# Kernel tuning notes

Hardware: AMD Instinct MI355X
Metric: run time of the kernel (lower is better)

Reference implementation:

```python
import jax, jax.numpy as jnp
import numpy as np

N_QUBITS = 4
N_QLAYERS = 2
NOISE = 0.05
LN_EPS = 1e-5
C64 = jnp.complex64

PX = jnp.array([[0, 1], [1, 0]], C64)
PY = jnp.array([[0, -1j], [1j, 0]], C64)
PZ = jnp.array([[1, 0], [0, -1]], C64)
CNOT = jnp.array([[1, 0, 0, 0], [0, 1, 0, 0], [0, 0, 0, 1], [0, 0, 1, 0]], C64).reshape(2, 2, 2, 2)


def _rx(t):
    c = jnp.cos(t / 2).astype(C64)
    s = jnp.sin(t / 2).astype(C64)
    return jnp.stack([jnp.stack([c, -1j * s], -1), jnp.stack([-1j * s, c], -1)], -2)


def _ry(t):
    c = jnp.cos(t / 2).astype(C64)
    s = jnp.sin(t / 2).astype(C64)
    return jnp.stack([jnp.stack([c, -s], -1), jnp.stack([s, c], -1)], -2)


def _rz(t):
    e = jnp.exp(-0.5j * t.astype(C64))
    z = jnp.zeros_like(e)
    return jnp.stack([jnp.stack([e, z], -1), jnp.stack([z, jnp.conj(e)], -1)], -2)


def _apply_1q(rho, U, q):
    # rho: [B] + [2]*8 (row qubit axes 1..4, col qubit axes 5..8); U: [2,2] or [B,2,2]
    r = jnp.moveaxis(rho, 1 + q, 1)
    r = jnp.einsum('bij,bj...->bi...', U, r) if U.ndim == 3 else jnp.einsum('ij,bj...->bi...', U, r)
    r = jnp.moveaxis(r, 1, 1 + q)
    r = jnp.moveaxis(r, 5 + q, -1)
    Uc = jnp.conj(U)
    r = jnp.einsum('b...j,bij->b...i', r, Uc) if U.ndim == 3 else jnp.einsum('b...j,ij->b...i', r, Uc)
    return jnp.moveaxis(r, -1, 5 + q)


def _apply_cnot(rho, c, t):
    r = jnp.moveaxis(rho, (1 + c, 1 + t), (1, 2))
    r = jnp.einsum('ABij,bij...->bAB...', CNOT, r)
    r = jnp.moveaxis(r, (1, 2), (1 + c, 1 + t))
    r = jnp.moveaxis(r, (5 + c, 5 + t), (-2, -1))
    r = jnp.einsum('b...ij,ABij->b...AB', r, jnp.conj(CNOT))
    return jnp.moveaxis(r, (-2, -1), (5 + c, 5 + t))


def _depolarize_all(rho, p):
    # rho -> (1-p) rho + p/3 (X rho X + Y rho Y + Z rho Z) on every qubit
    for q in range(N_QUBITS):
        rho = (1 - p) * rho + (p / 3) * (_apply_1q(rho, PX, q) + _apply_1q(rho, PY, q) + _apply_1q(rho, PZ, q))
    return rho


def _circuit(angles, w):
    # angles: [B,4] float, w: [2,4] float -> expval PauliZ per qubit: [B,4] float
    B = angles.shape[0]
    rho = jnp.zeros((B, 16, 16), C64).at[:, 0, 0].set(1.0).reshape((B,) + (2,) * 8)
    for i in range(N_QUBITS):
        rho = _apply_1q(rho, _rx(angles[:, i]), i)
        rho = _apply_1q(rho, _rz(angles[:, i]), i)
    for i in range(N_QUBITS):
        rho = _apply_1q(rho, _rx(w[0, i]), i)
        rho = _apply_1q(rho, _rz(w[1, i]), i)
    if NOISE > 0:
        rho = _depolarize_all(rho, NOISE)
    for l in range(1, N_QLAYERS):
        for i in range(N_QUBITS):
            rho = _apply_cnot(rho, i, (i + 1) % N_QUBITS)
            rho = _apply_1q(rho, _ry(w[l, i]), i)
            rho = _apply_1q(rho, _rz(w[l, i]), i)
        if NOISE > 0:
            rho = _depolarize_all(rho, NOISE)
    diag = jnp.real(jnp.diagonal(rho.reshape(B, 16, 16), axis1=1, axis2=2))  # [B,16]
    bits = (jnp.arange(16)[:, None] >> jnp.arange(N_QUBITS - 1, -1, -1)[None, :]) & 1
    signs = (1 - 2 * bits).astype(jnp.float32)  # [16,4]
    return diag @ signs


def setup_inputs() -> dict:
    key = jax.random.key(0)
    ks = jax.random.split(key, 4)
    B, D = 65536, 256
    x = jax.random.normal(ks[0], (B, D), jnp.float32)
    W_in = jax.random.normal(ks[1], (N_QUBITS, D), jnp.float32) * (1.0 / np.sqrt(D))
    b_in = jnp.zeros((N_QUBITS,), jnp.float32)
    gamma = jnp.ones((N_QUBITS,), jnp.float32)
    beta = jnp.zeros((N_QUBITS,), jnp.float32)
    qweights = jax.random.uniform(ks[2], (N_QLAYERS, N_QUBITS), jnp.float32, 0.0, 2.0 * np.pi)
    W_out = jax.random.normal(ks[3], (D, N_QUBITS), jnp.float32) * 0.5
    b_out = jnp.zeros((D,), jnp.float32)
    return dict(x=x, W_in=W_in, b_in=b_in, gamma=gamma, beta=beta, qweights=qweights, W_out=W_out, b_out=b_out)


def reference(x, W_in, b_in, gamma, beta, qweights, W_out, b_out):
    xp = jnp.tanh(x @ W_in.T + b_in)
    mu = jnp.mean(xp, -1, keepdims=True)
    var = jnp.mean((xp - mu) ** 2, -1, keepdims=True)
    angles = (xp - mu) / jnp.sqrt(var + LN_EPS) * gamma + beta  # timestep = 0.0
    z = _circuit(angles, qweights)
    out = z @ W_out.T + b_out
    return x + out  # residual: input_dim == output_dim
```

## Files before the change

### kernel.cpp

```cpp
#include <hip/hip_runtime.h>
#include <math.h>

#define DIM 256

__global__ void qc_setup_kernel(const float* __restrict__ qw, float* __restrict__ T)
{
  __shared__ float Vr[16][16], Vi[16][16];
  __shared__ float Or[16][16], Oi[16][16];
  const int tid = threadIdx.x;
  const int r = tid >> 4, c = tid & 15;

  Vr[r][c] = (r == c) ? 1.0f : 0.0f;
  Vi[r][c] = 0.0f;
  __syncthreads();

  #pragma unroll 1
  for (int i = 0; i < 4; ++i) {
    const int cm = 8 >> i;
    const int tm = 8 >> ((i + 1) & 3);
    {
      const int k = (r & cm) ? (r ^ tm) : r;
      const float nr = Vr[k][c], ni = Vi[k][c];
      __syncthreads();
      Vr[r][c] = nr; Vi[r][c] = ni;
      __syncthreads();
    }
    const float w  = qw[4 + i];
    const float ch = cosf(0.5f * w), sh = sinf(0.5f * w);
    {
      const int m = 8 >> i;
      const int r0 = r & ~m, r1 = r | m;
      float u0, u1;
      if (r & m) { u0 = sh; u1 = ch; } else { u0 = ch; u1 = -sh; }
      const float nr = u0 * Vr[r0][c] + u1 * Vr[r1][c];
      const float ni = u0 * Vi[r0][c] + u1 * Vi[r1][c];
      __syncthreads();
      Vr[r][c] = nr; Vi[r][c] = ni;
      __syncthreads();
    }
    {
      const int m = 8 >> i;
      const float pr = ch;
      const float pi = (r & m) ? sh : -sh;
      const float vr = Vr[r][c], vi = Vi[r][c];
      Vr[r][c] = pr * vr - pi * vi;
      Vi[r][c] = pr * vi + pi * vr;
      __syncthreads();
    }
  }

  const int q  = blockIdx.x;
  const int zm = 8 >> q;
  float orr = 0.0f, oii = 0.0f;
  for (int k = 0; k < 16; ++k) {
    const float sgn = (k & zm) ? -1.0f : 1.0f;
    const float ar = Vr[k][r], ai = -Vi[k][r];
    const float br = Vr[k][c], bi = Vi[k][c];
    orr += sgn * (ar * br - ai * bi);
    oii += sgn * (ar * bi + ai * br);
  }
  __syncthreads();
  Or[r][c] = orr; Oi[r][c] = oii;
  __syncthreads();

  const float sdep = 1.0f - 4.0f * 0.05f / 3.0f;
  const int p0 = tid >> 6, p1 = (tid >> 4) & 3, p2 = (tid >> 2) & 3, p3 = tid & 3;
  float tr = 0.0f;
  for (int n = 0; n < 16; ++n) {
    int m = n;
    float fr = 1.0f, fi = 0.0f;
    #pragma unroll
    for (int i2 = 0; i2 < 4; ++i2) {
      const int a   = (n >> (3 - i2)) & 1;
      const int pi_ = (i2 == 0) ? p0 : (i2 == 1) ? p1 : (i2 == 2) ? p2 : p3;
      if (pi_ == 1) {
        m ^= (8 >> i2);
      } else if (pi_ == 2) {
        m ^= (8 >> i2);
        const float s2  = a ? 1.0f : -1.0f;
        const float nfr = -fi * s2, nfi = fr * s2;
        fr = nfr; fi = nfi;
      } else if (pi_ == 3) {
        if (a) { fr = -fr; fi = -fi; }
      }
    }
    tr += fr * Or[m][n] - fi * Oi[m][n];
  }
  const int nnz = (p0 != 0) + (p1 != 0) + (p2 != 0) + (p3 != 0);
  float scale = 1.0f / 16.0f;
  for (int e = 0; e <= nnz; ++e) scale *= sdep;
  T[q * 256 + tid] = tr * scale;
}

__global__ __launch_bounds__(512)
__attribute__((amdgpu_waves_per_eu(4, 8)))
void qlayer_main_kernel(
    const float* __restrict__ x,
    const float* __restrict__ Win,
    const float* __restrict__ b_in,
    const float* __restrict__ gamma,
    const float* __restrict__ beta,
    const float* __restrict__ qw,
    const float* __restrict__ Wout,
    const float* __restrict__ b_out,
    const float* __restrict__ M,
    float* __restrict__ out,
    int B)
{
  __shared__ float accs[64][4];
  __shared__ float zz[64][4];

  const int tid  = threadIdx.x;
  const int lane = tid & 63;
  const int wv   = tid >> 6;
  const int lrow0 = wv * 8;
  const size_t grow0 = (size_t)blockIdx.x * 64 + lrow0;

  float4 winf[4];
  #pragma unroll
  for (int q = 0; q < 4; ++q)
    winf[q] = *reinterpret_cast<const float4*>(&Win[q * 256 + lane * 4]);

  float4 xr[8];
  #pragma unroll
  for (int i = 0; i < 8; ++i)
    xr[i] = *reinterpret_cast<const float4*>(&x[(grow0 + i) * DIM + lane * 4]);

  #pragma unroll
  for (int p = 0; p < 4; ++p) {
    float aA[4], aB[4];
    const float4 xa = xr[p * 2], xb = xr[p * 2 + 1];
    #pragma unroll
    for (int q = 0; q < 4; ++q) {
      aA[q] = xa.x * winf[q].x + xa.y * winf[q].y + xa.z * winf[q].z + xa.w * winf[q].w;
      aB[q] = xb.x * winf[q].x + xb.y * winf[q].y + xb.z * winf[q].z + xb.w * winf[q].w;
    }
    #pragma unroll
    for (int q = 0; q < 4; ++q) {
      aA[q] += __shfl_xor(aA[q], 32, 64);
      aB[q] += __shfl_xor(aB[q], 32, 64);
      aA[q] = (lane < 32) ? aA[q] : aB[q];
    }
    #pragma unroll
    for (int off = 1; off < 32; off <<= 1) {
      #pragma unroll
      for (int q = 0; q < 4; ++q) aA[q] += __shfl_xor(aA[q], off, 64);
    }
    if ((lane & 31) == 0) {
      const int lr = lrow0 + p * 2 + (lane >> 5);
      *reinterpret_cast<float4*>(&accs[lr][0]) = make_float4(aA[0], aA[1], aA[2], aA[3]);
    }
  }
  __syncthreads();

  if (tid < 64) {
    const float4 av = *reinterpret_cast<const float4*>(&accs[tid][0]);
    const float aq[4] = {av.x, av.y, av.z, av.w};

    float xp[4];
    #pragma unroll
    for (int q = 0; q < 4; ++q) {
      const float e = __expf(2.0f * (aq[q] + b_in[q]));
      xp[q] = 1.0f - __fdividef(2.0f, e + 1.0f);
    }
    const float mu = 0.25f * (xp[0] + xp[1] + xp[2] + xp[3]);
    const float d0 = xp[0] - mu, d1 = xp[1] - mu, d2 = xp[2] - mu, d3 = xp[3] - mu;
    const float var = 0.25f * (d0 * d0 + d1 * d1 + d2 * d2 + d3 * d3);
    const float inv = rsqrtf(var + 1e-5f);

    float A0[4], A1[4], A2[4], A3[4];
    #pragma unroll
    for (int i = 0; i < 4; ++i) {
      const float w0 = qw[i], w1 = qw[4 + i];
      const float cwa = cosf(w0), swa = sinf(w0);
      const float cwb = cosf(w1), swb = sinf(w1);
      const float ang = ((i == 0 ? d0 : i == 1 ? d1 : i == 2 ? d2 : d3) * inv) * gamma[i] + beta[i];
      float sn, cs;
      __sincosf(ang, &sn, &cs);
      const float ax = sn * sn;
      const float ay = -sn * cs;
      const float az = cs;
      const float ay2 = ay * cwa - az * swa;
      const float az2 = ay * swa + az * cwa;
      const float Axv = ax * cwb - ay2 * swb;
      const float Ayv = ax * swb + ay2 * cwb;
      float* dst = (i == 0) ? A0 : (i == 1) ? A1 : (i == 2) ? A2 : A3;
      dst[0] = 1.0f; dst[1] = Axv; dst[2] = Ayv; dst[3] = az2;
    }

    float v[16];
    #pragma unroll
    for (int a = 0; a < 4; ++a)
      #pragma unroll
      for (int b = 0; b < 4; ++b)
        v[a * 4 + b] = A2[a] * A3[b];

    float z[4];
    #pragma unroll
    for (int q = 0; q < 4; ++q) {
      float zq = 0.0f;
      #pragma unroll
      for (int j = 0; j < 16; ++j) {
        const float* Mr = &M[(q * 16 + j) * 16];
        float w = 0.0f;
        #pragma unroll
        for (int k = 0; k < 16; ++k) w += Mr[k] * v[k];
        zq += (A0[j >> 2] * A1[j & 3]) * w;
      }
      z[q] = zq;
    }
    *reinterpret_cast<float4*>(&zz[tid][0]) = make_float4(z[0], z[1], z[2], z[3]);
  }
  __syncthreads();

  float4 woutf[4];
  #pragma unroll
  for (int j = 0; j < 4; ++j)
    woutf[j] = *reinterpret_cast<const float4*>(&Wout[(lane * 4 + j) * 4]);
  const float4 boutf = *reinterpret_cast<const float4*>(&b_out[lane * 4]);

  #pragma unroll
  for (int i = 0; i < 8; ++i) {
    const float4 zv = *reinterpret_cast<const float4*>(&zz[lrow0 + i][0]);
    const float4 xv = xr[i];
    float4 o;
    o.x = xv.x + boutf.x + zv.x * woutf[0].x + zv.y * woutf[0].y + zv.z * woutf[0].z + zv.w * woutf[0].w;
    o.y = xv.y + boutf.y + zv.x * woutf[1].x + zv.y * woutf[1].y + zv.z * woutf[1].z + zv.w * woutf[1].w;
    o.z = xv.z + boutf.z + zv.x * woutf[2].x + zv.y * woutf[2].y + zv.z * woutf[2].z + zv.w * woutf[2].w;
    o.w = xv.w + boutf.w + zv.x * woutf[3].x + zv.y * woutf[3].y + zv.z * woutf[3].z + zv.w * woutf[3].w;
    *reinterpret_cast<float4*>(&out[(grow0 + i) * DIM + lane * 4]) = o;
  }
}

extern "C" void kernel_launch(void* const* d_in, const int* in_sizes, int n_in,
                              void* d_out, int out_size, void* d_ws, size_t ws_size,
                              hipStream_t stream)
{
  const float* x     = (const float*)d_in[0];
  const float* Win   = (const float*)d_in[1];
  const float* b_in  = (const float*)d_in[2];
  const float* gamma = (const float*)d_in[3];
  const float* beta  = (const float*)d_in[4];
  const float* qw    = (const float*)d_in[5];
  const float* Wout  = (const float*)d_in[6];
  const float* b_out = (const float*)d_in[7];
  float* out = (float*)d_out;
  float* T   = (float*)d_ws;
  const int B = in_sizes[0] / DIM;

  hipLaunchKernelGGL(qc_setup_kernel, dim3(4), dim3(256), 0, stream, qw, T);

  const int nblocks = B / 64;
  hipLaunchKernelGGL(qlayer_main_kernel, dim3(nblocks), dim3(512), 0, stream,
                     x, Win, b_in, gamma, beta, qw, Wout, b_out, T, out, B);
}
```

Measured before the change: 53.40 us.

## Split fused main kernel into projection, circuit, and epilogue kernels

New measurement: 64.66 us. 21.1% more time.

```diff
diff --git a/kernel.cpp b/kernel.cpp
--- a/kernel.cpp
+++ b/kernel.cpp
@@ -92,144 +92,152 @@
   T[q * 256 + tid] = tr * scale;
 }
 
-__global__ __launch_bounds__(512)
-__attribute__((amdgpu_waves_per_eu(4, 8)))
-void qlayer_main_kernel(
+__global__ __launch_bounds__(256) void k1_angles(
     const float* __restrict__ x,
     const float* __restrict__ Win,
+    float* __restrict__ acc,
+    int B)
+{
+  const int lane = threadIdx.x & 63;
+  const int wid  = blockIdx.x * (blockDim.x >> 6) + (threadIdx.x >> 6);
+  const int nw   = gridDim.x * (blockDim.x >> 6);
+
+  float4 winf[4];
+  #pragma unroll
+  for (int q = 0; q < 4; ++q)
+    winf[q] = *reinterpret_cast<const float4*>(&Win[q * 256 + lane * 4]);
+
+  const int npair = B >> 1;
+  #pragma unroll 1
+  for (int p = wid; p < npair; p += nw) {
+    const size_t base = (size_t)p * 2 * DIM + lane * 4;
+    const float4 xa = *reinterpret_cast<const float4*>(&x[base]);
+    const float4 xb = *reinterpret_cast<const float4*>(&x[base + DIM]);
+
+    float aA[4], aB[4];
+    #pragma unroll
+    for (int q = 0; q < 4; ++q) {
+      aA[q] = xa.x * winf[q].x + xa.y * winf[q].y + xa.z * winf[q].z + xa.w * winf[q].w;
+      aB[q] = xb.x * winf[q].x + xb.y * winf[q].y + xb.z * winf[q].z + xb.w * winf[q].w;
+    }
+    #pragma unroll
+    for (int q = 0; q < 4; ++q) {
+      aA[q] += __shfl_xor(aA[q], 32, 64);
+      aB[q] += __shfl_xor(aB[q], 32, 64);
+      aA[q] = (lane < 32) ? aA[q] : aB[q];
+    }
+    #pragma unroll
+    for (int off = 1; off < 32; off <<= 1) {
+      #pragma unroll
+      for (int q = 0; q < 4; ++q) aA[q] += __shfl_xor(aA[q], off, 64);
+    }
+    if ((lane & 31) == 0) {
+      const int row = p * 2 + (lane >> 5);
+      *reinterpret_cast<float4*>(&acc[(size_t)row * 4]) =
+          make_float4(aA[0], aA[1], aA[2], aA[3]);
+    }
+  }
+}
+
+__global__ __launch_bounds__(256) void k2_middle(
+    const float* __restrict__ acc,
     const float* __restrict__ b_in,
     const float* __restrict__ gamma,
     const float* __restrict__ beta,
     const float* __restrict__ qw,
+    const float* __restrict__ M,
+    float* __restrict__ z,
+    int B)
+{
+  const int g = blockIdx.x * blockDim.x + threadIdx.x;
+  if (g >= B) return;
+
+  const float4 av = *reinterpret_cast<const float4*>(&acc[(size_t)g * 4]);
+  const float aq[4] = {av.x, av.y, av.z, av.w};
+
+  float xp[4];
+  #pragma unroll
+  for (int q = 0; q < 4; ++q) {
+    const float e = __expf(2.0f * (aq[q] + b_in[q]));
+    xp[q] = 1.0f - __fdividef(2.0f, e + 1.0f);
+  }
+  const float mu = 0.25f * (xp[0] + xp[1] + xp[2] + xp[3]);
+  const float d0 = xp[0] - mu, d1 = xp[1] - mu, d2 = xp[2] - mu, d3 = xp[3] - mu;
+  const float var = 0.25f * (d0 * d0 + d1 * d1 + d2 * d2 + d3 * d3);
+  const float inv = rsqrtf(var + 1e-5f);
+
+  float A0[4], A1[4], A2[4], A3[4];
+  #pragma unroll
+  for (int i = 0; i < 4; ++i) {
+    const float w0 = qw[i], w1 = qw[4 + i];
+    const float cwa = cosf(w0), swa = sinf(w0);
+    const float cwb = cosf(w1), swb = sinf(w1);
+    const float ang = ((i == 0 ? d0 : i == 1 ? d1 : i == 2 ? d2 : d3) * inv) * gamma[i] + beta[i];
+    float sn, cs;
+    __sincosf(ang, &sn, &cs);
+    const float ax = sn * sn;
+    const float ay = -sn * cs;
+    const float az = cs;
+    const float ay2 = ay * cwa - az * swa;
+    const float az2 = ay * swa + az * cwa;
+    const float Axv = ax * cwb - ay2 * swb;
+    const float Ayv = ax * swb + ay2 * cwb;
+    float* dst = (i == 0) ? A0 : (i == 1) ? A1 : (i == 2) ? A2 : A3;
+    dst[0] = 1.0f; dst[1] = Axv; dst[2] = Ayv; dst[3] = az2;
+  }
+
+  float v[16];
+  #pragma unroll
+  for (int a = 0; a < 4; ++a)
+    #pragma unroll
+    for (int b = 0; b < 4; ++b)
+      v[a * 4 + b] = A2[a] * A3[b];
+
+  float zo[4];
+  #pragma unroll
+  for (int q = 0; q < 4; ++q) {
+    float zq = 0.0f;
+    #pragma unroll
+    for (int j = 0; j < 16; ++j) {
+      const float* Mr = &M[(q * 16 + j) * 16];
+      float w = 0.0f;
+      #pragma unroll
+      for (int k = 0; k < 16; ++k) w += Mr[k] * v[k];
+      zq += (A0[j >> 2] * A1[j & 3]) * w;
+    }
+    zo[q] = zq;
+  }
+  *reinterpret_cast<float4*>(&z[(size_t)g * 4]) =
+      make_float4(zo[0], zo[1], zo[2], zo[3]);
+}
+
+__global__ __launch_bounds__(256) void k3_epilogue(
+    const float* __restrict__ x,
+    const float* __restrict__ z,
     const float* __restrict__ Wout,
     const float* __restrict__ b_out,
-    const float* __restrict__ M,
     float* __restrict__ out,
     int B)
 {
-  __shared__ float accs[64][4];
-  __shared__ float zz[64][4];
-
-  const int tid  = threadIdx.x;
-  const int lane = tid & 63;
-  const int wv   = tid >> 6;
-  const int lrow0 = wv * 8;
-  const size_t grow0 = (size_t)blockIdx.x * 64 + lrow0;
-
-  float4 winf[4];
-  #pragma unroll
-  for (int q = 0; q < 4; ++q)
-    winf[q] = *reinterpret_cast<const float4*>(&Win[q * 256 + lane * 4]);
-
-  float4 xr[8];
-  #pragma unroll
-  for (int i = 0; i < 8; ++i)
-    xr[i] = *reinterpret_cast<const float4*>(&x[(grow0 + i) * DIM + lane * 4]);
-
-  #pragma unroll
-  for (int p = 0; p < 4; ++p) {
-    float aA[4], aB[4];
-    const float4 xa = xr[p * 2], xb = xr[p * 2 + 1];
-    #pragma unroll
-    for (int q = 0; q < 4; ++q) {
-      aA[q] = xa.x * winf[q].x + xa.y * winf[q].y + xa.z * winf[q].z + xa.w * winf[q].w;
-      aB[q] = xb.x * winf[q].x + xb.y * winf[q].y + xb.z * winf[q].z + xb.w * winf[q].w;
-    }
-    #pragma unroll
-    for (int q = 0; q < 4; ++q) {
-      aA[q] += __shfl_xor(aA[q], 32, 64);
-      aB[q] += __shfl_xor(aB[q], 32, 64);
-      aA[q] = (lane < 32) ? aA[q] : aB[q];
-    }
-    #pragma unroll
-    for (int off = 1; off < 32; off <<= 1) {
-      #pragma unroll
-      for (int q = 0; q < 4; ++q) aA[q] += __shfl_xor(aA[q], off, 64);
-    }
-    if ((lane & 31) == 0) {
-      const int lr = lrow0 + p * 2 + (lane >> 5);
-      *reinterpret_cast<float4*>(&accs[lr][0]) = make_float4(aA[0], aA[1], aA[2], aA[3]);
-    }
-  }
-  __syncthreads();
-
-  if (tid < 64) {
-    const float4 av = *reinterpret_cast<const float4*>(&accs[tid][0]);
-    const float aq[4] = {av.x, av.y, av.z, av.w};
-
-    float xp[4];
-    #pragma unroll
-    for (int q = 0; q < 4; ++q) {
-      const float e = __expf(2.0f * (aq[q] + b_in[q]));
-      xp[q] = 1.0f - __fdividef(2.0f, e + 1.0f);
-    }
-    const float mu = 0.25f * (xp[0] + xp[1] + xp[2] + xp[3]);
-    const float d0 = xp[0] - mu, d1 = xp[1] - mu, d2 = xp[2] - mu, d3 = xp[3] - mu;
-    const float var = 0.25f * (d0 * d0 + d1 * d1 + d2 * d2 + d3 * d3);
-    const float inv = rsqrtf(var + 1e-5f);
-
-    float A0[4], A1[4], A2[4], A3[4];
-    #pragma unroll
-    for (int i = 0; i < 4; ++i) {
-      const float w0 = qw[i], w1 = qw[4 + i];
-      const float cwa = cosf(w0), swa = sinf(w0);
-      const float cwb = cosf(w1), swb = sinf(w1);
-      const float ang = ((i == 0 ? d0 : i == 1 ? d1 : i == 2 ? d2 : d3) * inv) * gamma[i] + beta[i];
-      float sn, cs;
-      __sincosf(ang, &sn, &cs);
-      const float ax = sn * sn;
-      const float ay = -sn * cs;
-      const float az = cs;
-      const float ay2 = ay * cwa - az * swa;
-      const float az2 = ay * swa + az * cwa;
-      const float Axv = ax * cwb - ay2 * swb;
-      const float Ayv = ax * swb + ay2 * cwb;
-      float* dst = (i == 0) ? A0 : (i == 1) ? A1 : (i == 2) ? A2 : A3;
-      dst[0] = 1.0f; dst[1] = Axv; dst[2] = Ayv; dst[3] = az2;
-    }
-
-    float v[16];
-    #pragma unroll
-    for (int a = 0; a < 4; ++a)
-      #pragma unroll
-      for (int b = 0; b < 4; ++b)
-        v[a * 4 + b] = A2[a] * A3[b];
-
-    float z[4];
-    #pragma unroll
-    for (int q = 0; q < 4; ++q) {
-      float zq = 0.0f;
-      #pragma unroll
-      for (int j = 0; j < 16; ++j) {
-        const float* Mr = &M[(q * 16 + j) * 16];
-        float w = 0.0f;
-        #pragma unroll
-        for (int k = 0; k < 16; ++k) w += Mr[k] * v[k];
-        zq += (A0[j >> 2] * A1[j & 3]) * w;
-      }
-      z[q] = zq;
-    }
-    *reinterpret_cast<float4*>(&zz[tid][0]) = make_float4(z[0], z[1], z[2], z[3]);
-  }
-  __syncthreads();
-
-  float4 woutf[4];
-  #pragma unroll
-  for (int j = 0; j < 4; ++j)
-    woutf[j] = *reinterpret_cast<const float4*>(&Wout[(lane * 4 + j) * 4]);
-  const float4 boutf = *reinterpret_cast<const float4*>(&b_out[lane * 4]);
-
-  #pragma unroll
-  for (int i = 0; i < 8; ++i) {
-    const float4 zv = *reinterpret_cast<const float4*>(&zz[lrow0 + i][0]);
-    const float4 xv = xr[i];
-    float4 o;
-    o.x = xv.x + boutf.x + zv.x * woutf[0].x + zv.y * woutf[0].y + zv.z * woutf[0].z + zv.w * woutf[0].w;
-    o.y = xv.y + boutf.y + zv.x * woutf[1].x + zv.y * woutf[1].y + zv.z * woutf[1].z + zv.w * woutf[1].w;
-    o.z = xv.z + boutf.z + zv.x * woutf[2].x + zv.y * woutf[2].y + zv.z * woutf[2].z + zv.w * woutf[2].w;
-    o.w = xv.w + boutf.w + zv.x * woutf[3].x + zv.y * woutf[3].y + zv.z * woutf[3].z + zv.w * woutf[3].w;
-    *reinterpret_cast<float4*>(&out[(grow0 + i) * DIM + lane * 4]) = o;
-  }
+  const size_t g = (size_t)blockIdx.x * blockDim.x + threadIdx.x;
+  const int row = (int)(g >> 6);
+  const int c4  = (int)(g & 63);
+  if (row >= B) return;
+
+  const float4 xv = *reinterpret_cast<const float4*>(&x[g * 4]);
+  const float4 zv = *reinterpret_cast<const float4*>(&z[(size_t)row * 4]);
+  const float4 w0 = *reinterpret_cast<const float4*>(&Wout[(c4 * 4 + 0) * 4]);
+  const float4 w1 = *reinterpret_cast<const float4*>(&Wout[(c4 * 4 + 1) * 4]);
+  const float4 w2 = *reinterpret_cast<const float4*>(&Wout[(c4 * 4 + 2) * 4]);
+  const float4 w3 = *reinterpret_cast<const float4*>(&Wout[(c4 * 4 + 3) * 4]);
+  const float4 bv = *reinterpret_cast<const float4*>(&b_out[c4 * 4]);
+
+  float4 o;
+  o.x = xv.x + bv.x + zv.x * w0.x + zv.y * w0.y + zv.z * w0.z + zv.w * w0.w;
+  o.y = xv.y + bv.y + zv.x * w1.x + zv.y * w1.y + zv.z * w1.z + zv.w * w1.w;
+  o.z = xv.z + bv.z + zv.x * w2.x + zv.y * w2.y + zv.z * w2.z + zv.w * w2.w;
+  o.w = xv.w + bv.w + zv.x * w3.x + zv.y * w3.y + zv.z * w3.z + zv.w * w3.w;
+  *reinterpret_cast<float4*>(&out[g * 4]) = o;
 }
 
 extern "C" void kernel_launch(void* const* d_in, const int* in_sizes, int n_in,
@@ -245,12 +253,20 @@
   const float* Wout  = (const float*)d_in[6];
   const float* b_out = (const float*)d_in[7];
   float* out = (float*)d_out;
-  float* T   = (float*)d_ws;
   const int B = in_sizes[0] / DIM;
 
-  hipLaunchKernelGGL(qc_setup_kernel, dim3(4), dim3(256), 0, stream, qw, T);
-
-  const int nblocks = B / 64;
-  hipLaunchKernelGGL(qlayer_main_kernel, dim3(nblocks), dim3(512), 0, stream,
-                     x, Win, b_in, gamma, beta, qw, Wout, b_out, T, out, B);
-}
+  float* M   = (float*)d_ws;
+  float* acc = M + 1024;
+  float* zbuf = acc + (size_t)B * 4;
+
+  hipLaunchKernelGGL(qc_setup_kernel, dim3(4), dim3(256), 0, stream, qw, M);
+
+  hipLaunchKernelGGL(k1_angles, dim3(2048), dim3(256), 0, stream, x, Win, acc, B);
+
+  hipLaunchKernelGGL(k2_middle, dim3((B + 255) / 256), dim3(256), 0, stream,
+                     acc, b_in, gamma, beta, qw, M, zbuf, B);
+
+  const size_t nf4 = (size_t)B * 64;
+  hipLaunchKernelGGL(k3_epilogue, dim3((unsigned)((nf4 + 255) / 256)), dim3(256),
+                     0, stream, x, zbuf, Wout, b_out, out, B);
+}
```

## Stage x tile transposed in shared memory and compute input projection per-thread

Applied to the files above, without the earlier changes.

New measurement: 70.15 us. +31.4%, slower.

```diff
diff --git a/kernel.cpp b/kernel.cpp
--- a/kernel.cpp
+++ b/kernel.cpp
@@ -2,6 +2,7 @@
 #include <math.h>
 
 #define DIM 256
+#define TILE 32
 
 __global__ void qc_setup_kernel(const float* __restrict__ qw, float* __restrict__ T)
 {
@@ -92,9 +93,7 @@
   T[q * 256 + tid] = tr * scale;
 }
 
-__global__ __launch_bounds__(512)
-__attribute__((amdgpu_waves_per_eu(4, 8)))
-void qlayer_main_kernel(
+__global__ __launch_bounds__(256) void qlayer_main_kernel(
     const float* __restrict__ x,
     const float* __restrict__ Win,
     const float* __restrict__ b_in,
@@ -107,60 +106,46 @@
     float* __restrict__ out,
     int B)
 {
-  __shared__ float accs[64][4];
-  __shared__ float zz[64][4];
+  __shared__ float xs[256][33];
+  __shared__ float accs[32][4];
+  __shared__ float zz[32][4];
 
   const int tid  = threadIdx.x;
+  const int w    = tid >> 6;
   const int lane = tid & 63;
-  const int wv   = tid >> 6;
-  const int lrow0 = wv * 8;
-  const size_t grow0 = (size_t)blockIdx.x * 64 + lrow0;
-
-  float4 winf[4];
+  const int r0   = blockIdx.x * TILE;
+
   #pragma unroll
-  for (int q = 0; q < 4; ++q)
-    winf[q] = *reinterpret_cast<const float4*>(&Win[q * 256 + lane * 4]);
-
-  float4 xr[8];
-  #pragma unroll
-  for (int i = 0; i < 8; ++i)
-    xr[i] = *reinterpret_cast<const float4*>(&x[(grow0 + i) * DIM + lane * 4]);
-
-  #pragma unroll
-  for (int p = 0; p < 4; ++p) {
-    float aA[4], aB[4];
-    const float4 xa = xr[p * 2], xb = xr[p * 2 + 1];
+  for (int i = 0; i < 8; ++i) {
+    const int row = i * 4 + w;
+    const float4 v = *reinterpret_cast<const float4*>(
+        &x[(size_t)(r0 + row) * DIM + lane * 4]);
+    xs[lane * 4 + 0][row] = v.x;
+    xs[lane * 4 + 1][row] = v.y;
+    xs[lane * 4 + 2][row] = v.z;
+    xs[lane * 4 + 3][row] = v.w;
+  }
+  __syncthreads();
+
+  {
+    const int l = lane & 31;
+    const float* Wq = Win + w * 256;
+    float a = 0.0f;
+    #pragma unroll 8
+    for (int k = 0; k < 256; ++k)
+      a += xs[k][l] * Wq[k];
+    if (lane < 32) accs[l][w] = a;
+  }
+  __syncthreads();
+
+  if (tid < 32) {
+    const float4 av = *reinterpret_cast<const float4*>(&accs[tid][0]);
+    const float aqv[4] = {av.x, av.y, av.z, av.w};
+
+    float xp[4];
     #pragma unroll
     for (int q = 0; q < 4; ++q) {
-      aA[q] = xa.x * winf[q].x + xa.y * winf[q].y + xa.z * winf[q].z + xa.w * winf[q].w;
-      aB[q] = xb.x * winf[q].x + xb.y * winf[q].y + xb.z * winf[q].z + xb.w * winf[q].w;
-    }
-    #pragma unroll
-    for (int q = 0; q < 4; ++q) {
-      aA[q] += __shfl_xor(aA[q], 32, 64);
-      aB[q] += __shfl_xor(aB[q], 32, 64);
-      aA[q] = (lane < 32) ? aA[q] : aB[q];
-    }
-    #pragma unroll
-    for (int off = 1; off < 32; off <<= 1) {
-      #pragma unroll
-      for (int q = 0; q < 4; ++q) aA[q] += __shfl_xor(aA[q], off, 64);
-    }
-    if ((lane & 31) == 0) {
-      const int lr = lrow0 + p * 2 + (lane >> 5);
-      *reinterpret_cast<float4*>(&accs[lr][0]) = make_float4(aA[0], aA[1], aA[2], aA[3]);
-    }
-  }
-  __syncthreads();
-
-  if (tid < 64) {
-    const float4 av = *reinterpret_cast<const float4*>(&accs[tid][0]);
-    const float aq[4] = {av.x, av.y, av.z, av.w};
-
-    float xp[4];
-    #pragma unroll
-    for (int q = 0; q < 4; ++q) {
-      const float e = __expf(2.0f * (aq[q] + b_in[q]));
+      const float e = __expf(2.0f * (aqv[q] + b_in[q]));
       xp[q] = 1.0f - __fdividef(2.0f, e + 1.0f);
     }
     const float mu = 0.25f * (xp[0] + xp[1] + xp[2] + xp[3]);
@@ -202,10 +187,10 @@
       #pragma unroll
       for (int j = 0; j < 16; ++j) {
         const float* Mr = &M[(q * 16 + j) * 16];
-        float w = 0.0f;
+        float ww = 0.0f;
         #pragma unroll
-        for (int k = 0; k < 16; ++k) w += Mr[k] * v[k];
-        zq += (A0[j >> 2] * A1[j & 3]) * w;
+        for (int k = 0; k < 16; ++k) ww += Mr[k] * v[k];
+        zq += (A0[j >> 2] * A1[j & 3]) * ww;
       }
       z[q] = zq;
     }
@@ -221,14 +206,18 @@
 
   #pragma unroll
   for (int i = 0; i < 8; ++i) {
-    const float4 zv = *reinterpret_cast<const float4*>(&zz[lrow0 + i][0]);
-    const float4 xv = xr[i];
+    const int row = i * 4 + w;
+    const float4 zv = *reinterpret_cast<const float4*>(&zz[row][0]);
+    const float xv0 = xs[lane * 4 + 0][row];
+    const float xv1 = xs[lane * 4 + 1][row];
+    const float xv2 = xs[lane * 4 + 2][row];
+    const float xv3 = xs[lane * 4 + 3][row];
     float4 o;
-    o.x = xv.x + boutf.x + zv.x * woutf[0].x + zv.y * woutf[0].y + zv.z * woutf[0].z + zv.w * woutf[0].w;
-    o.y = xv.y + boutf.y + zv.x * woutf[1].x + zv.y * woutf[1].y + zv.z * woutf[1].z + zv.w * woutf[1].w;
-    o.z = xv.z + boutf.z + zv.x * woutf[2].x + zv.y * woutf[2].y + zv.z * woutf[2].z + zv.w * woutf[2].w;
-    o.w = xv.w + boutf.w + zv.x * woutf[3].x + zv.y * woutf[3].y + zv.z * woutf[3].z + zv.w * woutf[3].w;
-    *reinterpret_cast<float4*>(&out[(grow0 + i) * DIM + lane * 4]) = o;
+    o.x = xv0 + boutf.x + zv.x * woutf[0].x + zv.y * woutf[0].y + zv.z * woutf[0].z + zv.w * woutf[0].w;
+    o.y = xv1 + boutf.y + zv.x * woutf[1].x + zv.y * woutf[1].y + zv.z * woutf[1].z + zv.w * woutf[1].w;
+    o.z = xv2 + boutf.z + zv.x * woutf[2].x + zv.y * woutf[2].y + zv.z * woutf[2].z + zv.w * woutf[2].w;
+    o.w = xv3 + boutf.w + zv.x * woutf[3].x + zv.y * woutf[3].y + zv.z * woutf[3].z + zv.w * woutf[3].w;
+    *reinterpret_cast<float4*>(&out[(size_t)(r0 + row) * DIM + lane * 4]) = o;
   }
 }
 
@@ -245,12 +234,12 @@
   const float* Wout  = (const float*)d_in[6];
   const float* b_out = (const float*)d_in[7];
   float* out = (float*)d_out;
-  float* T   = (float*)d_ws;
+  float* M   = (float*)d_ws;
   const int B = in_sizes[0] / DIM;
 
-  hipLaunchKernelGGL(qc_setup_kernel, dim3(4), dim3(256), 0, stream, qw, T);
-
-  const int nblocks = B / 64;
-  hipLaunchKernelGGL(qlayer_main_kernel, dim3(nblocks), dim3(512), 0, stream,
-                     x, Win, b_in, gamma, beta, qw, Wout, b_out, T, out, B);
+  hipLaunchKernelGGL(qc_setup_kernel, dim3(4), dim3(256), 0, stream, qw, M);
+
+  const int nblocks = B / TILE;
+  hipLaunchKernelGGL(qlayer_main_kernel, dim3(nblocks), dim3(256), 0, stream,
+                     x, Win, b_in, gamma, beta, qw, Wout, b_out, M, out, B);
 }
```
